# Optimization experiments

Hardware: AMD Instinct MI355X
Metric: run time of the kernel (lower is better)

## Reference

```python
import jax, jax.numpy as jnp
import numpy as np

USER_NUM = 100000
ITEM_NUM = 150000
N_NODES = USER_NUM + ITEM_NUM
EMB = 64
N_LAYERS = 3
N_EDGES = 1200000


def setup_inputs() -> dict:
    key = jax.random.key(0)
    k1, k2, k3, k4, k5 = jax.random.split(key, 5)
    user_emb = jax.random.normal(k1, (USER_NUM, EMB), dtype=jnp.float32) * 0.1
    item_emb = jax.random.normal(k2, (ITEM_NUM, EMB), dtype=jnp.float32) * 0.1
    adj_rows = jax.random.randint(k3, (N_EDGES,), 0, N_NODES, dtype=jnp.int32)
    adj_cols = jax.random.randint(k4, (N_EDGES,), 0, N_NODES, dtype=jnp.int32)
    # normalized-adjacency-like positive values
    adj_vals = jax.random.uniform(k5, (N_EDGES,), dtype=jnp.float32) * 0.1
    return {"user_emb": user_emb, "item_emb": item_emb,
            "adj_rows": adj_rows, "adj_cols": adj_cols, "adj_vals": adj_vals}


def _spmm(rows, cols, vals, embeds):
    # out[r] += vals[e] * embeds[cols[e]]  — torch.spmm(adj, embeds) with COO adj
    msgs = vals[:, None] * embeds[cols]           # [E, d]
    return jax.ops.segment_sum(msgs, rows, num_segments=N_NODES)


def reference(user_emb, item_emb, adj_rows, adj_cols, adj_vals):
    # forward_graphcl: concat embeddings, n_layers spmm hops, sum all hop outputs
    embeds = jnp.concatenate([user_emb, item_emb], axis=0)  # [N, d]
    main = embeds
    cur = embeds
    for _ in range(N_LAYERS):
        cur = _spmm(adj_rows, adj_cols, adj_vals, cur)
        main = main + cur
    return main
```

## Files before the change

### kernel.cpp

```cpp
#include <hip/hip_runtime.h>
#include <hip/hip_fp16.h>

#define USER_NUM 100000
#define ITEM_NUM 150000
#define N_NODES  250000
#define EMB      64
#define N_EDGES  1200000
#define N_ELEM   (N_NODES * EMB)

#define NBLK1 512
#define NBUCK 245
#define CAP   8192
#define TB1   4096
#define INIT_BLOCKS 977

typedef float f4 __attribute__((ext_vector_type(4)));
typedef int   i4 __attribute__((ext_vector_type(4)));

__device__ __forceinline__ void wavescan256(int* __restrict__ s, int t)
{
    if (t < 64) {
        i4 v = *(i4*)(s + 4 * t);
        v.y += v.x; v.z += v.y; v.w += v.z;
        int x = v.w;
#pragma unroll
        for (int off = 1; off < 64; off <<= 1) {
            int y = __shfl_up(x, off);
            if (t >= off) x += y;
        }
        int excl = x - v.w;
        v.x += excl; v.y += excl; v.z += excl; v.w += excl;
        *(i4*)(s + 4 * t) = v;
    }
}

__global__ __launch_bounds__(1024) void bin_kernel(
    const int* __restrict__ rows, const int* __restrict__ cols,
    const float* __restrict__ vals,
    int* __restrict__ chunkcur, int* __restrict__ bucket_cnt,
    int2* __restrict__ tmp)
{
    __shared__ __align__(16) int scnt[256];
    __shared__ __align__(16) int spref[256];
    __shared__ __align__(16) int sexcl[256];
    __shared__ int  schunk[NBUCK];
    __shared__ unsigned char sbuck[TB1];
    __shared__ int2 tilebuf[TB1];

    int b = blockIdx.x, t = threadIdx.x;
    int e0 = (int)((long long)b * N_EDGES / NBLK1);
    int e1 = (int)((long long)(b + 1) * N_EDGES / NBLK1);

    int er[3], ec[3]; float ev[3];
#pragma unroll
    for (int k = 0; k < 3; ++k) {
        int e = e0 + t + k * 1024;
        bool ok = (e < e1);
        er[k] = ok ? rows[e] : -1;
        ec[k] = ok ? cols[e] : 0;
        ev[k] = ok ? vals[e] : 0.0f;
    }

    if (t < 256) scnt[t] = 0;
    __syncthreads();
#pragma unroll
    for (int k = 0; k < 3; ++k)
        if (er[k] >= 0) atomicAdd(&scnt[er[k] >> 10], 1);
    __syncthreads();

    int realc = (t < NBUCK) ? scnt[t] : 0;
    int v     = (realc + 7) & ~7;
    if (t < 256) spref[t] = v;
    __syncthreads();
    wavescan256(spref, t);
    __syncthreads();
    int padded_total = spref[255];
    int excl = (t < 256) ? spref[t] - v : 0;
    if (t < 256) { sexcl[t] = excl; scnt[t] = excl; }
    if (t < NBUCK) {
        schunk[t] = (v > 0) ? atomicAdd(&chunkcur[t], v >> 3) : 0;
        if (realc > 0) atomicAdd(&bucket_cnt[t], realc);
        for (int k = realc; k < v; ++k) tilebuf[excl + k] = make_int2(-1, 0);
        for (int k = 0; k < v; ++k)     sbuck[excl + k] = (unsigned char)t;
    }
    __syncthreads();
#pragma unroll
    for (int k = 0; k < 3; ++k) {
        if (er[k] >= 0) {
            int lp = atomicAdd(&scnt[er[k] >> 10], 1);
            tilebuf[lp] = make_int2(((er[k] & 1023) << 18) | ec[k], __float_as_int(ev[k]));
        }
    }
    __syncthreads();
    for (int j = t; j < padded_total; j += 1024) {
        int lo = sbuck[j];
        tmp[(size_t)lo * CAP + schunk[lo] * 8 + (j - sexcl[lo])] = tilebuf[j];
    }
}

__global__ __launch_bounds__(1024) void place_init_kernel(
    const int* __restrict__ chunkcur, const int* __restrict__ bucket_cnt,
    const int2* __restrict__ tmp,
    int* __restrict__ row_ptr, int2* __restrict__ edges,
    const float* __restrict__ user, const float* __restrict__ item,
    __half* __restrict__ emb16)
{
    __shared__ __align__(16) int shist[1024];
    __shared__ __align__(16) int swave[256];
    __shared__ int2 sstage[CAP];

    int t = threadIdx.x;
    if (blockIdx.x >= NBUCK) {
        int gi = (blockIdx.x - NBUCK) * 1024 + t;
        if (gi < N_ELEM / 16) {
            int base = gi * 16;
            const int UE = USER_NUM * EMB;
            const f4* src = (base < UE) ? (const f4*)(user + base)
                                        : (const f4*)(item + (base - UE));
            f4 f0 = __builtin_nontemporal_load(src);
            f4 f1 = __builtin_nontemporal_load(src + 1);
            f4 f2 = __builtin_nontemporal_load(src + 2);
            f4 f3 = __builtin_nontemporal_load(src + 3);
            union { i4 v; __half2 h[4]; } a, bq;
            a.h[0] = __float22half2_rn(make_float2(f0.x, f0.y));
            a.h[1] = __float22half2_rn(make_float2(f0.z, f0.w));
            a.h[2] = __float22half2_rn(make_float2(f1.x, f1.y));
            a.h[3] = __float22half2_rn(make_float2(f1.z, f1.w));
            bq.h[0] = __float22half2_rn(make_float2(f2.x, f2.y));
            bq.h[1] = __float22half2_rn(make_float2(f2.z, f2.w));
            bq.h[2] = __float22half2_rn(make_float2(f3.x, f3.y));
            bq.h[3] = __float22half2_rn(make_float2(f3.z, f3.w));
            ((i4*)(emb16 + base))[0] = a.v;
            ((i4*)(emb16 + base))[1] = bq.v;
        }
        return;
    }

    int b = blockIdx.x;
    int nrec = chunkcur[b] * 8;
    const int2* src = tmp + (size_t)b * CAP;

    int2 recs[8];
#pragma unroll
    for (int k = 0; k < 8; ++k) {
        int j = t + k * 1024;
        recs[k] = (j < nrec) ? src[j] : make_int2(-1, 0);
    }

    if (t < 256) swave[t] = (t < NBUCK) ? bucket_cnt[t] : 0;
    shist[t] = 0;
    __syncthreads();
    wavescan256(swave, t);
    __syncthreads();
    int bb  = (b == 0) ? 0 : swave[b - 1];
    int cnt = swave[b] - bb;
    __syncthreads();

#pragma unroll
    for (int k = 0; k < 8; ++k)
        if (recs[k].x != -1) atomicAdd(&shist[recs[k].x >> 18], 1);
    __syncthreads();

    int h0 = 0, h1 = 0, h2 = 0, h3 = 0, sum = 0;
    if (t < 256) {
        h0 = shist[4 * t]; h1 = shist[4 * t + 1];
        h2 = shist[4 * t + 2]; h3 = shist[4 * t + 3];
        sum = h0 + h1 + h2 + h3;
        swave[t] = sum;
    }
    __syncthreads();
    wavescan256(swave, t);
    __syncthreads();
    if (t < 256) {
        int base = bb + swave[t] - sum;
        shist[4 * t]     = base;
        shist[4 * t + 1] = base + h0;
        shist[4 * t + 2] = base + h0 + h1;
        shist[4 * t + 3] = base + h0 + h1 + h2;
    }
    __syncthreads();
    {
        int idx = b * 1024 + t;
        if (idx < N_NODES) row_ptr[idx] = shist[t];
    }
    if (b == 0 && t == 0) row_ptr[N_NODES] = N_EDGES;
    __syncthreads();
#pragma unroll
    for (int k = 0; k < 8; ++k) {
        if (recs[k].x != -1) {
            int lp = atomicAdd(&shist[recs[k].x >> 18], 1) - bb;
            sstage[lp] = make_int2(recs[k].x & 0x3FFFF, recs[k].y);
        }
    }
    __syncthreads();
    for (int j = t; j < cnt; j += 1024)
        edges[bb + j] = sstage[j];
}

template <int MODE>
__global__ __launch_bounds__(256) void spmm_kernel(
    const int* __restrict__ row_ptr, const int2* __restrict__ edges,
    const __half* __restrict__ in16, const __half* __restrict__ emb16,
    const __half* __restrict__ cur1,
    float* __restrict__ out, __half* __restrict__ cur_out)
{
    int t = blockIdx.x * blockDim.x + threadIdx.x;
    int r = t >> 4;
    int l = t & 15;
    if (r >= N_NODES) return;
    int start = row_ptr[r];
    int end   = row_ptr[r + 1];
    int idx   = r * EMB + 4 * l;

    union { int2 i; __half2 h[2]; } pe, p1, p2;
    if (MODE == 1) {
        pe.i = *(const int2*)(emb16 + idx);
        p1.i = *(const int2*)(cur1 + idx);
        p2.i = *(const int2*)(in16 + idx);
    }

    float ax = 0.f, ay = 0.f, az = 0.f, aw = 0.f;
    for (int j = start; j < end; j += 8) {
        int2 e[8];
#pragma unroll
        for (int k = 0; k < 8; ++k) e[k] = edges[j + k];
#pragma unroll
        for (int k = 0; k < 8; ++k) {
            bool ok = (j + k < end);
            int   c = ok ? e[k].x : 0;
            float v = ok ? __int_as_float(e[k].y) : 0.0f;
            union { int2 i; __half2 h[2]; } g;
            g.i = *(const int2*)(in16 + c * EMB + 4 * l);
            float2 x0 = __half22float2(g.h[0]);
            float2 x1 = __half22float2(g.h[1]);
            ax += v * x0.x; ay += v * x0.y;
            az += v * x1.x; aw += v * x1.y;
        }
    }

    if (MODE == 0) {
        union { int2 i; __half2 h[2]; } o;
        o.h[0] = __float22half2_rn(make_float2(ax, ay));
        o.h[1] = __float22half2_rn(make_float2(az, aw));
        *(int2*)(cur_out + idx) = o.i;
    } else {
        float2 e0 = __half22float2(pe.h[0]), e1 = __half22float2(pe.h[1]);
        float2 c0 = __half22float2(p1.h[0]), c1 = __half22float2(p1.h[1]);
        float2 d0 = __half22float2(p2.h[0]), d1 = __half22float2(p2.h[1]);
        float4 o = make_float4(e0.x + c0.x + d0.x + ax,
                               e0.y + c0.y + d0.y + ay,
                               e1.x + c1.x + d1.x + az,
                               e1.y + c1.y + d1.y + aw);
        *(float4*)(out + idx) = o;
    }
}

extern "C" void kernel_launch(void* const* d_in, const int* in_sizes, int n_in,
                              void* d_out, int out_size, void* d_ws, size_t ws_size,
                              hipStream_t stream) {
    const float* user = (const float*)d_in[0];
    const float* item = (const float*)d_in[1];
    const int*   rows = (const int*)d_in[2];
    const int*   cols = (const int*)d_in[3];
    const float* vals = (const float*)d_in[4];
    float*       out  = (float*)d_out;

    char* p = (char*)d_ws;
    __half* emb16   = (__half*)p;  p += (size_t)N_ELEM * 2;
    __half* cur1    = (__half*)p;  p += (size_t)N_ELEM * 2;
    __half* cur2    = (__half*)p;  p += (size_t)N_ELEM * 2;
    int2*   tmp     = (int2*)p;    p += (size_t)NBUCK * CAP * 8;
    int2*   edges   = (int2*)p;    p += (size_t)(N_EDGES + 32) * 8;
    int*    row_ptr = (int*)p;     p += 1000448;
    int*    bucket_cnt = (int*)p;  p += 1024;
    int*    chunkcur   = (int*)p;  p += 1024;

    hipMemsetAsync(bucket_cnt, 0, 2048, stream);

    bin_kernel<<<NBLK1, 1024, 0, stream>>>(rows, cols, vals, chunkcur, bucket_cnt, tmp);
    place_init_kernel<<<NBUCK + INIT_BLOCKS, 1024, 0, stream>>>(
        chunkcur, bucket_cnt, tmp, row_ptr, edges, user, item, emb16);

    const int spmm_blocks = (N_NODES * 16 + 255) / 256;
    spmm_kernel<0><<<spmm_blocks, 256, 0, stream>>>(row_ptr, edges, emb16, emb16, cur1, out, cur1);
    spmm_kernel<0><<<spmm_blocks, 256, 0, stream>>>(row_ptr, edges, cur1, emb16, cur1, out, cur2);
    spmm_kernel<1><<<spmm_blocks, 256, 0, stream>>>(row_ptr, edges, cur2, emb16, cur1, out, nullptr);
}
```

Baseline: 261.5 us.

## Replace atomic chunk binning with per-block prefix tables and fixed bucket slots

The binning kernel now writes each block's bucket-sorted edges contiguously and records per-bucket counts and offsets in transposed tables. This replaces the global atomic chunk allocation, the padding and the memset. The placement kernel gathers each bucket's segments from all 512 blocks, two threads per segment, and writes edges into fixed CAP-sized slots per bucket. Row extents are stored as start/end pairs, so no global prefix over buckets is needed. The spmm loop skips gathers for padded lanes instead of loading row 0. In exchange, the gather reads are scattered and small, and the edges array has gaps between buckets. The tmp buffer is aliased with cur2, which is safe because tmp is consumed before cur2 is written.

```diff
diff --git a/kernel.cpp b/kernel.cpp
--- a/kernel.cpp
+++ b/kernel.cpp
@@ -11,7 +11,7 @@
 #define NBLK1 512
 #define NBUCK 245
 #define CAP   8192
-#define TB1   4096
+#define TMPB  2560
 #define INIT_BLOCKS 977
 
 typedef float f4 __attribute__((ext_vector_type(4)));
@@ -37,19 +37,17 @@
 __global__ __launch_bounds__(1024) void bin_kernel(
     const int* __restrict__ rows, const int* __restrict__ cols,
     const float* __restrict__ vals,
-    int* __restrict__ chunkcur, int* __restrict__ bucket_cnt,
+    int* __restrict__ pcntT, int* __restrict__ sprefT,
     int2* __restrict__ tmp)
 {
     __shared__ __align__(16) int scnt[256];
     __shared__ __align__(16) int spref[256];
-    __shared__ __align__(16) int sexcl[256];
-    __shared__ int  schunk[NBUCK];
-    __shared__ unsigned char sbuck[TB1];
-    __shared__ int2 tilebuf[TB1];
+    __shared__ int2 tilebuf[TMPB];
 
     int b = blockIdx.x, t = threadIdx.x;
     int e0 = (int)((long long)b * N_EDGES / NBLK1);
     int e1 = (int)((long long)(b + 1) * N_EDGES / NBLK1);
+    int tot = e1 - e0;
 
     int er[3], ec[3]; float ev[3];
 #pragma unroll
@@ -68,20 +66,16 @@
         if (er[k] >= 0) atomicAdd(&scnt[er[k] >> 10], 1);
     __syncthreads();
 
-    int realc = (t < NBUCK) ? scnt[t] : 0;
-    int v     = (realc + 7) & ~7;
-    if (t < 256) spref[t] = v;
+    int realc = (t < 256) ? scnt[t] : 0;
+    if (t < 256) spref[t] = realc;
     __syncthreads();
     wavescan256(spref, t);
     __syncthreads();
-    int padded_total = spref[255];
-    int excl = (t < 256) ? spref[t] - v : 0;
-    if (t < 256) { sexcl[t] = excl; scnt[t] = excl; }
-    if (t < NBUCK) {
-        schunk[t] = (v > 0) ? atomicAdd(&chunkcur[t], v >> 3) : 0;
-        if (realc > 0) atomicAdd(&bucket_cnt[t], realc);
-        for (int k = realc; k < v; ++k) tilebuf[excl + k] = make_int2(-1, 0);
-        for (int k = 0; k < v; ++k)     sbuck[excl + k] = (unsigned char)t;
+    if (t < 256) {
+        int excl = spref[t] - realc;
+        pcntT[t * 512 + b]  = realc;
+        sprefT[t * 512 + b] = excl;
+        scnt[t] = excl;
     }
     __syncthreads();
 #pragma unroll
@@ -92,16 +86,14 @@
         }
     }
     __syncthreads();
-    for (int j = t; j < padded_total; j += 1024) {
-        int lo = sbuck[j];
-        tmp[(size_t)lo * CAP + schunk[lo] * 8 + (j - sexcl[lo])] = tilebuf[j];
-    }
+    for (int j = t; j < tot; j += 1024)
+        tmp[(size_t)b * TMPB + j] = tilebuf[j];
 }
 
 __global__ __launch_bounds__(1024) void place_init_kernel(
-    const int* __restrict__ chunkcur, const int* __restrict__ bucket_cnt,
+    const int* __restrict__ pcntT, const int* __restrict__ sprefT,
     const int2* __restrict__ tmp,
-    int* __restrict__ row_ptr, int2* __restrict__ edges,
+    int2* __restrict__ row_se, int2* __restrict__ edges,
     const float* __restrict__ user, const float* __restrict__ item,
     __half* __restrict__ emb16)
 {
@@ -136,29 +128,17 @@
         return;
     }
 
-    int b = blockIdx.x;
-    int nrec = chunkcur[b] * 8;
-    const int2* src = tmp + (size_t)b * CAP;
-
-    int2 recs[8];
-#pragma unroll
-    for (int k = 0; k < 8; ++k) {
-        int j = t + k * 1024;
-        recs[k] = (j < nrec) ? src[j] : make_int2(-1, 0);
-    }
-
-    if (t < 256) swave[t] = (t < NBUCK) ? bucket_cnt[t] : 0;
+    int B  = blockIdx.x;
+    int bp = t >> 1;
+    int half = t & 1;
+    int seg_s = sprefT[B * 512 + bp];
+    int seg_l = pcntT[B * 512 + bp];
+    const int2* tsrc = tmp + (size_t)bp * TMPB + seg_s;
+
     shist[t] = 0;
     __syncthreads();
-    wavescan256(swave, t);
-    __syncthreads();
-    int bb  = (b == 0) ? 0 : swave[b - 1];
-    int cnt = swave[b] - bb;
-    __syncthreads();
-
-#pragma unroll
-    for (int k = 0; k < 8; ++k)
-        if (recs[k].x != -1) atomicAdd(&shist[recs[k].x >> 18], 1);
+    for (int i = half; i < seg_l; i += 2)
+        atomicAdd(&shist[tsrc[i].x >> 18], 1);
     __syncthreads();
 
     int h0 = 0, h1 = 0, h2 = 0, h3 = 0, sum = 0;
@@ -172,34 +152,34 @@
     wavescan256(swave, t);
     __syncthreads();
     if (t < 256) {
-        int base = bb + swave[t] - sum;
-        shist[4 * t]     = base;
-        shist[4 * t + 1] = base + h0;
-        shist[4 * t + 2] = base + h0 + h1;
-        shist[4 * t + 3] = base + h0 + h1 + h2;
-    }
-    __syncthreads();
-    {
-        int idx = b * 1024 + t;
-        if (idx < N_NODES) row_ptr[idx] = shist[t];
-    }
-    if (b == 0 && t == 0) row_ptr[N_NODES] = N_EDGES;
-    __syncthreads();
-#pragma unroll
-    for (int k = 0; k < 8; ++k) {
-        if (recs[k].x != -1) {
-            int lp = atomicAdd(&shist[recs[k].x >> 18], 1) - bb;
-            sstage[lp] = make_int2(recs[k].x & 0x3FFFF, recs[k].y);
-        }
-    }
-    __syncthreads();
-    for (int j = t; j < cnt; j += 1024)
-        edges[bb + j] = sstage[j];
+        int a0 = swave[t] - sum;
+        int a1 = a0 + h0, a2 = a1 + h1, a3 = a2 + h2, a4 = a3 + h3;
+        shist[4 * t]     = a0;
+        shist[4 * t + 1] = a1;
+        shist[4 * t + 2] = a2;
+        shist[4 * t + 3] = a3;
+        int gb = B * CAP;
+        int r0 = B * 1024 + 4 * t;
+        if (r0 + 0 < N_NODES) row_se[r0 + 0] = make_int2(gb + a0, gb + a1);
+        if (r0 + 1 < N_NODES) row_se[r0 + 1] = make_int2(gb + a1, gb + a2);
+        if (r0 + 2 < N_NODES) row_se[r0 + 2] = make_int2(gb + a2, gb + a3);
+        if (r0 + 3 < N_NODES) row_se[r0 + 3] = make_int2(gb + a3, gb + a4);
+    }
+    __syncthreads();
+    for (int i = half; i < seg_l; i += 2) {
+        int2 rec = tsrc[i];
+        int  lp  = atomicAdd(&shist[rec.x >> 18], 1);
+        sstage[lp] = make_int2(rec.x & 0x3FFFF, rec.y);
+    }
+    __syncthreads();
+    int total = shist[1023];
+    for (int j = t; j < total; j += 1024)
+        edges[(size_t)B * CAP + j] = sstage[j];
 }
 
 template <int MODE>
 __global__ __launch_bounds__(256) void spmm_kernel(
-    const int* __restrict__ row_ptr, const int2* __restrict__ edges,
+    const int2* __restrict__ row_se, const int2* __restrict__ edges,
     const __half* __restrict__ in16, const __half* __restrict__ emb16,
     const __half* __restrict__ cur1,
     float* __restrict__ out, __half* __restrict__ cur_out)
@@ -208,8 +188,8 @@
     int r = t >> 4;
     int l = t & 15;
     if (r >= N_NODES) return;
-    int start = row_ptr[r];
-    int end   = row_ptr[r + 1];
+    int2 se   = row_se[r];
+    int start = se.x, end = se.y;
     int idx   = r * EMB + 4 * l;
 
     union { int2 i; __half2 h[2]; } pe, p1, p2;
@@ -226,15 +206,16 @@
         for (int k = 0; k < 8; ++k) e[k] = edges[j + k];
 #pragma unroll
         for (int k = 0; k < 8; ++k) {
-            bool ok = (j + k < end);
-            int   c = ok ? e[k].x : 0;
-            float v = ok ? __int_as_float(e[k].y) : 0.0f;
-            union { int2 i; __half2 h[2]; } g;
-            g.i = *(const int2*)(in16 + c * EMB + 4 * l);
-            float2 x0 = __half22float2(g.h[0]);
-            float2 x1 = __half22float2(g.h[1]);
-            ax += v * x0.x; ay += v * x0.y;
-            az += v * x1.x; aw += v * x1.y;
+            if (j + k < end) {
+                int   c = e[k].x;
+                float v = __int_as_float(e[k].y);
+                union { int2 i; __half2 h[2]; } g;
+                g.i = *(const int2*)(in16 + c * EMB + 4 * l);
+                float2 x0 = __half22float2(g.h[0]);
+                float2 x1 = __half22float2(g.h[1]);
+                ax += v * x0.x; ay += v * x0.y;
+                az += v * x1.x; aw += v * x1.y;
+            }
         }
     }
 
@@ -266,23 +247,22 @@
     float*       out  = (float*)d_out;
 
     char* p = (char*)d_ws;
-    __half* emb16   = (__half*)p;  p += (size_t)N_ELEM * 2;
-    __half* cur1    = (__half*)p;  p += (size_t)N_ELEM * 2;
-    __half* cur2    = (__half*)p;  p += (size_t)N_ELEM * 2;
-    int2*   tmp     = (int2*)p;    p += (size_t)NBUCK * CAP * 8;
-    int2*   edges   = (int2*)p;    p += (size_t)(N_EDGES + 32) * 8;
-    int*    row_ptr = (int*)p;     p += 1000448;
-    int*    bucket_cnt = (int*)p;  p += 1024;
-    int*    chunkcur   = (int*)p;  p += 1024;
-
-    hipMemsetAsync(bucket_cnt, 0, 2048, stream);
-
-    bin_kernel<<<NBLK1, 1024, 0, stream>>>(rows, cols, vals, chunkcur, bucket_cnt, tmp);
+    __half* emb16  = (__half*)p;  p += (size_t)N_ELEM * 2;
+    __half* cur1   = (__half*)p;  p += (size_t)N_ELEM * 2;
+    int2*   edges  = (int2*)p;    p += (size_t)NBUCK * CAP * 8 + 256;
+    int2*   row_se = (int2*)p;    p += (size_t)N_NODES * 8 + 256;
+    char*   xbase  = p;
+    __half* cur2   = (__half*)xbase;
+    int2*   tmp    = (int2*)xbase;
+    int*    pcntT  = (int*)(xbase + (size_t)NBLK1 * TMPB * 8);
+    int*    sprefT = pcntT + 256 * 512;
+
+    bin_kernel<<<NBLK1, 1024, 0, stream>>>(rows, cols, vals, pcntT, sprefT, tmp);
     place_init_kernel<<<NBUCK + INIT_BLOCKS, 1024, 0, stream>>>(
-        chunkcur, bucket_cnt, tmp, row_ptr, edges, user, item, emb16);
+        pcntT, sprefT, tmp, row_se, edges, user, item, emb16);
 
     const int spmm_blocks = (N_NODES * 16 + 255) / 256;
-    spmm_kernel<0><<<spmm_blocks, 256, 0, stream>>>(row_ptr, edges, emb16, emb16, cur1, out, cur1);
-    spmm_kernel<0><<<spmm_blocks, 256, 0, stream>>>(row_ptr, edges, cur1, emb16, cur1, out, cur2);
-    spmm_kernel<1><<<spmm_blocks, 256, 0, stream>>>(row_ptr, edges, cur2, emb16, cur1, out, nullptr);
-}
+    spmm_kernel<0><<<spmm_blocks, 256, 0, stream>>>(row_se, edges, emb16, emb16, cur1, out, cur1);
+    spmm_kernel<0><<<spmm_blocks, 256, 0, stream>>>(row_se, edges, cur1, emb16, cur1, out, cur2);
+    spmm_kernel<1><<<spmm_blocks, 256, 0, stream>>>(row_se, edges, cur2, emb16, cur1, out, nullptr);
+}
```

Result: slower. 295.1 us (+12.8%).
